# Kernel optimization log

Hardware: AMD Instinct MI355X
Metric: run time of the kernel (lower is better)

## Reference

```python
import jax, jax.numpy as jnp
import numpy as np

EPS = 1e-8
NEG_INF = -9e15  # matches torch masked_fill value


def setup_inputs() -> dict:
    key = jax.random.key(0)
    k1, k2 = jax.random.split(key)
    B, D = 4096, 512
    p1 = jax.random.normal(k1, (B, D), dtype=jnp.float32)
    p2 = jax.random.normal(k2, (B, D), dtype=jnp.float32)
    return {"p1": p1, "p2": p2}


def reference(p1, p2):
    # NT-Xent / InfoNCE loss as in SimCLR_MODEL.contrastive_loss (temperature = 1).
    z = jnp.concatenate([p1, p2], axis=0)              # [N, D], N = 2B
    # cosine similarity == GEMM of L2-normalized rows (torch eps clamp = 1e-8)
    zn = z / jnp.maximum(jnp.linalg.norm(z, axis=-1, keepdims=True), EPS)
    sim = zn @ zn.T                                     # [N, N]
    N = sim.shape[0]
    idx = jnp.arange(N)
    sim = sim.at[idx, idx].set(NEG_INF)                 # mask self-similarity
    # positive pair of row i is row (i + N/2) mod N (eye rolled by N/2)
    pos = sim[idx, (idx + N // 2) % N]                  # [N]
    nll = -pos + jax.nn.logsumexp(sim, axis=-1)
    return jnp.mean(nll)
```

## Files before the change

kernel.cpp:

```cpp
#include <hip/hip_runtime.h>
#include <hip/hip_bf16.h>
#include <math.h>

#define N_TOT 8192
#define HALF_N 4096
#define D_DIM 512
#define BM 128
#define BK 64
#define NTILES 2080

typedef float f32x4_t __attribute__((ext_vector_type(4)));

typedef __attribute__((address_space(1))) unsigned int g_u32;
typedef __attribute__((address_space(3))) unsigned int l_u32;

__global__ __launch_bounds__(256) void k_normalize(
    const float* __restrict__ p1, const float* __restrict__ p2,
    unsigned char* __restrict__ zf8, float* __restrict__ rowsum,
    float* __restrict__ out)
{
    const int w = threadIdx.x >> 6;
    const int lane = threadIdx.x & 63;
    const int row = blockIdx.x * 4 + w;

    if (threadIdx.x < 4) rowsum[blockIdx.x * 4 + threadIdx.x] = 0.0f;
    if (blockIdx.x == 0 && threadIdx.x == 0) out[0] = 0.0f;

    const float* src = (row < HALF_N) ? p1 + (size_t)row * D_DIM
                                      : p2 + (size_t)(row - HALF_N) * D_DIM;
    float4 a = *(const float4*)(src + lane * 4);
    float4 b = *(const float4*)(src + 256 + lane * 4);
    float s = a.x*a.x + a.y*a.y + a.z*a.z + a.w*a.w
            + b.x*b.x + b.y*b.y + b.z*b.z + b.w*b.w;
    #pragma unroll
    for (int m = 1; m < 64; m <<= 1) s += __shfl_xor(s, m, 64);
    float inv = 1.0f / fmaxf(sqrtf(s), 1e-8f);

    int pk0 = __builtin_amdgcn_cvt_pk_fp8_f32(a.x * inv, a.y * inv, 0, false);
    pk0     = __builtin_amdgcn_cvt_pk_fp8_f32(a.z * inv, a.w * inv, pk0, true);
    int pk1 = __builtin_amdgcn_cvt_pk_fp8_f32(b.x * inv, b.y * inv, 0, false);
    pk1     = __builtin_amdgcn_cvt_pk_fp8_f32(b.z * inv, b.w * inv, pk1, true);

    unsigned char* dst = zf8 + (size_t)row * D_DIM;
    *(int*)(dst + lane * 4) = pk0;
    *(int*)(dst + 256 + lane * 4) = pk1;
}

__global__ __launch_bounds__(256) void k_gemm(
    const unsigned char* __restrict__ zf8,
    float* __restrict__ rowsum, float* __restrict__ pos)
{
    __shared__ __align__(16) unsigned char As[BM * BK];
    __shared__ __align__(16) unsigned char Bs[BM * BK];

    const int tid = threadIdx.x;
    const int lane = tid & 63;
    const int w = tid >> 6;
    const int wr = w >> 1, wc = w & 1;
    const int q = lane >> 4, l15 = lane & 15;

    const int t = blockIdx.x;
    int bi = (int)((sqrtf(8.0f * (float)t + 1.0f) - 1.0f) * 0.5f);
    while ((bi + 1) * (bi + 2) / 2 <= t) ++bi;
    while (bi * (bi + 1) / 2 > t) --bi;
    const int bx = bi;
    const int by = t - bi * (bi + 1) / 2;
    const bool isDiag = (bx == by);
    const bool hasPos = (bx - by == 32);
    const int rowBase = by * BM;
    const int colBase = bx * BM;

    const int ci0 = tid;
    const int ci1 = 256 + tid;
    const int r0 = ci0 >> 2, cc0 = ci0 & 3;
    const int r1 = ci1 >> 2, cc1 = ci1 & 3;
    const int gc0 = cc0 ^ ((r0 >> 1) & 3);
    const int gc1 = cc1 ^ ((r1 >> 1) & 3);

    f32x4_t acc[4][4] = {};

    for (int kb = 0; kb < D_DIM; kb += BK) {
        const unsigned char* ga0 = zf8 + (size_t)(rowBase + r0) * D_DIM + kb + gc0 * 16;
        const unsigned char* ga1 = zf8 + (size_t)(rowBase + r1) * D_DIM + kb + gc1 * 16;
        const unsigned char* gb0 = zf8 + (size_t)(colBase + r0) * D_DIM + kb + gc0 * 16;
        const unsigned char* gb1 = zf8 + (size_t)(colBase + r1) * D_DIM + kb + gc1 * 16;
        __builtin_amdgcn_global_load_lds((const g_u32*)ga0, (l_u32*)&As[ci0 * 16], 16, 0, 0);
        __builtin_amdgcn_global_load_lds((const g_u32*)ga1, (l_u32*)&As[ci1 * 16], 16, 0, 0);
        __builtin_amdgcn_global_load_lds((const g_u32*)gb0, (l_u32*)&Bs[ci0 * 16], 16, 0, 0);
        __builtin_amdgcn_global_load_lds((const g_u32*)gb1, (l_u32*)&Bs[ci1 * 16], 16, 0, 0);
        __syncthreads();

        long long af[2][4], bfr[2][4];
        #pragma unroll
        for (int h = 0; h < 2; h++) {
            #pragma unroll
            for (int i = 0; i < 4; i++) {
                const int ra = wr * 64 + i * 16 + l15;
                const int rb = wc * 64 + i * 16 + l15;
                const int ca = ((h * 2 + (q >> 1)) ^ ((ra >> 1) & 3)) * 16 + (q & 1) * 8;
                const int cb = ((h * 2 + (q >> 1)) ^ ((rb >> 1) & 3)) * 16 + (q & 1) * 8;
                af[h][i]  = *(const long long*)&As[ra * BK + ca];
                bfr[h][i] = *(const long long*)&Bs[rb * BK + cb];
            }
        }
        #pragma unroll
        for (int h = 0; h < 2; h++)
            #pragma unroll
            for (int i = 0; i < 4; i++)
                #pragma unroll
                for (int j = 0; j < 4; j++)
                    acc[i][j] = __builtin_amdgcn_mfma_f32_16x16x32_fp8_fp8(
                        af[h][i], bfr[h][j], acc[i][j], 0, 0, 0);
        __syncthreads();
    }

    float colacc[4] = {0.f, 0.f, 0.f, 0.f};
    #pragma unroll
    for (int i = 0; i < 4; i++) {
        #pragma unroll
        for (int r = 0; r < 4; r++) {
            const int row = rowBase + wr * 64 + i * 16 + q * 4 + r;
            float rs = 0.0f;
            #pragma unroll
            for (int j = 0; j < 4; j++) {
                const int col = colBase + wc * 64 + j * 16 + l15;
                const float c = acc[i][j][r];
                float e = __expf(c);
                if (isDiag && col == row) e = 0.0f;
                rs += e;
                colacc[j] += e;
                if (hasPos && col == row + HALF_N) { pos[row] = c; pos[col] = c; }
            }
            rs += __shfl_xor(rs, 1); rs += __shfl_xor(rs, 2);
            rs += __shfl_xor(rs, 4); rs += __shfl_xor(rs, 8);
            if (l15 == 0) atomicAdd(&rowsum[row], rs);
        }
    }
    if (!isDiag) {
        #pragma unroll
        for (int j = 0; j < 4; j++) {
            float cs = colacc[j];
            cs += __shfl_xor(cs, 16);
            cs += __shfl_xor(cs, 32);
            if (q == 0) atomicAdd(&rowsum[colBase + wc * 64 + j * 16 + l15], cs);
        }
    }
}

__global__ __launch_bounds__(256) void k_finalize(
    const float* __restrict__ rowsum, const float* __restrict__ pos,
    float* __restrict__ out)
{
    const int t = threadIdx.x;
    const int i = blockIdx.x * 256 + t;
    float s = logf(rowsum[i]) - pos[i];
    #pragma unroll
    for (int m = 1; m < 64; m <<= 1) s += __shfl_xor(s, m, 64);
    __shared__ float red[4];
    if ((t & 63) == 0) red[t >> 6] = s;
    __syncthreads();
    if (t == 0)
        atomicAdd(out, (red[0] + red[1] + red[2] + red[3]) * (1.0f / (float)N_TOT));
}

extern "C" void kernel_launch(void* const* d_in, const int* in_sizes, int n_in,
                              void* d_out, int out_size, void* d_ws, size_t ws_size,
                              hipStream_t stream) {
    const float* p1 = (const float*)d_in[0];
    const float* p2 = (const float*)d_in[1];

    unsigned char* zf8 = (unsigned char*)d_ws;
    float* rowsum = (float*)((char*)d_ws + (size_t)N_TOT * D_DIM);
    float* pos    = rowsum + N_TOT;
    float* outp   = (float*)d_out;

    k_normalize<<<N_TOT / 4, 256, 0, stream>>>(p1, p2, zf8, rowsum, outp);
    k_gemm<<<NTILES, 256, 0, stream>>>(zf8, rowsum, pos);
    k_finalize<<<N_TOT / 256, 256, 0, stream>>>(rowsum, pos, outp);
}
```

Baseline: 109.2 us.

## Double-buffer LDS tiles in fp8 GEMM to prefetch the next K-slice

Splits the shared-memory A/B tiles into two buffers. The next K-slice is issued with global_load_lds while MFMAs run on the current slice, and one barrier per iteration replaces two. Precomputed base pointers and a fully unrolled K loop cut address arithmetic. launch_bounds(256,3) asks for three resident blocks per CU to help hide latency, which the doubled LDS use and register pressure could work against.

Result: no change. 108.9 us (-0.3%).

```diff
diff --git a/kernel.cpp b/kernel.cpp
--- a/kernel.cpp
+++ b/kernel.cpp
@@ -7,6 +7,7 @@
 #define D_DIM 512
 #define BM 128
 #define BK 64
+#define NKIT (D_DIM / BK)
 #define NTILES 2080
 
 typedef float f32x4_t __attribute__((ext_vector_type(4)));
@@ -46,12 +47,12 @@
     *(int*)(dst + 256 + lane * 4) = pk1;
 }
 
-__global__ __launch_bounds__(256) void k_gemm(
+__global__ __launch_bounds__(256, 3) void k_gemm(
     const unsigned char* __restrict__ zf8,
     float* __restrict__ rowsum, float* __restrict__ pos)
 {
-    __shared__ __align__(16) unsigned char As[BM * BK];
-    __shared__ __align__(16) unsigned char Bs[BM * BK];
+    __shared__ __align__(16) unsigned char As[2][BM * BK];
+    __shared__ __align__(16) unsigned char Bs[2][BM * BK];
 
     const int tid = threadIdx.x;
     const int lane = tid & 63;
@@ -77,18 +78,31 @@
     const int gc0 = cc0 ^ ((r0 >> 1) & 3);
     const int gc1 = cc1 ^ ((r1 >> 1) & 3);
 
+    const unsigned char* gA0 = zf8 + (size_t)(rowBase + r0) * D_DIM + gc0 * 16;
+    const unsigned char* gA1 = zf8 + (size_t)(rowBase + r1) * D_DIM + gc1 * 16;
+    const unsigned char* gB0 = zf8 + (size_t)(colBase + r0) * D_DIM + gc0 * 16;
+    const unsigned char* gB1 = zf8 + (size_t)(colBase + r1) * D_DIM + gc1 * 16;
+
     f32x4_t acc[4][4] = {};
 
-    for (int kb = 0; kb < D_DIM; kb += BK) {
-        const unsigned char* ga0 = zf8 + (size_t)(rowBase + r0) * D_DIM + kb + gc0 * 16;
-        const unsigned char* ga1 = zf8 + (size_t)(rowBase + r1) * D_DIM + kb + gc1 * 16;
-        const unsigned char* gb0 = zf8 + (size_t)(colBase + r0) * D_DIM + kb + gc0 * 16;
-        const unsigned char* gb1 = zf8 + (size_t)(colBase + r1) * D_DIM + kb + gc1 * 16;
-        __builtin_amdgcn_global_load_lds((const g_u32*)ga0, (l_u32*)&As[ci0 * 16], 16, 0, 0);
-        __builtin_amdgcn_global_load_lds((const g_u32*)ga1, (l_u32*)&As[ci1 * 16], 16, 0, 0);
-        __builtin_amdgcn_global_load_lds((const g_u32*)gb0, (l_u32*)&Bs[ci0 * 16], 16, 0, 0);
-        __builtin_amdgcn_global_load_lds((const g_u32*)gb1, (l_u32*)&Bs[ci1 * 16], 16, 0, 0);
+    __builtin_amdgcn_global_load_lds((const g_u32*)gA0, (l_u32*)&As[0][ci0 * 16], 16, 0, 0);
+    __builtin_amdgcn_global_load_lds((const g_u32*)gA1, (l_u32*)&As[0][ci1 * 16], 16, 0, 0);
+    __builtin_amdgcn_global_load_lds((const g_u32*)gB0, (l_u32*)&Bs[0][ci0 * 16], 16, 0, 0);
+    __builtin_amdgcn_global_load_lds((const g_u32*)gB1, (l_u32*)&Bs[0][ci1 * 16], 16, 0, 0);
+
+    #pragma unroll
+    for (int it = 0; it < NKIT; it++) {
+        const int cur = it & 1;
         __syncthreads();
+
+        if (it + 1 < NKIT) {
+            const int kb = (it + 1) * BK;
+            const int nxt = 1 - cur;
+            __builtin_amdgcn_global_load_lds((const g_u32*)(gA0 + kb), (l_u32*)&As[nxt][ci0 * 16], 16, 0, 0);
+            __builtin_amdgcn_global_load_lds((const g_u32*)(gA1 + kb), (l_u32*)&As[nxt][ci1 * 16], 16, 0, 0);
+            __builtin_amdgcn_global_load_lds((const g_u32*)(gB0 + kb), (l_u32*)&Bs[nxt][ci0 * 16], 16, 0, 0);
+            __builtin_amdgcn_global_load_lds((const g_u32*)(gB1 + kb), (l_u32*)&Bs[nxt][ci1 * 16], 16, 0, 0);
+        }
 
         long long af[2][4], bfr[2][4];
         #pragma unroll
@@ -99,8 +113,8 @@
                 const int rb = wc * 64 + i * 16 + l15;
                 const int ca = ((h * 2 + (q >> 1)) ^ ((ra >> 1) & 3)) * 16 + (q & 1) * 8;
                 const int cb = ((h * 2 + (q >> 1)) ^ ((rb >> 1) & 3)) * 16 + (q & 1) * 8;
-                af[h][i]  = *(const long long*)&As[ra * BK + ca];
-                bfr[h][i] = *(const long long*)&Bs[rb * BK + cb];
+                af[h][i]  = *(const long long*)&As[cur][ra * BK + ca];
+                bfr[h][i] = *(const long long*)&Bs[cur][rb * BK + cb];
             }
         }
         #pragma unroll
@@ -111,7 +125,6 @@
                 for (int j = 0; j < 4; j++)
                     acc[i][j] = __builtin_amdgcn_mfma_f32_16x16x32_fp8_fp8(
                         af[h][i], bfr[h][j], acc[i][j], 0, 0, 0);
-        __syncthreads();
     }
 
     float colacc[4] = {0.f, 0.f, 0.f, 0.f};
```

## Load MFMA fragments directly from global in pre-permuted fp8 layout, drop LDS staging

Applied to the files above, without the earlier changes.

The normalize kernel now writes fp8 rows in a permuted byte order within each 64-byte chunk, so each lane's two MFMA k-slices sit in one contiguous 16-byte run. The GEMM kernel drops shared memory and barriers and reads its A/B fragments straight from global memory with 16-byte vector loads, prefetching the next k-block in registers while the current one is multiplied. This removes LDS traffic and __syncthreads, but each wave now loads its own fragments, so data shared between waves is fetched redundantly through L1/L2 and register pressure goes up.

New measurement: 155.1 us. +41.9%, slower.

```diff
diff --git a/kernel.cpp b/kernel.cpp
--- a/kernel.cpp
+++ b/kernel.cpp
@@ -6,13 +6,11 @@
 #define HALF_N 4096
 #define D_DIM 512
 #define BM 128
-#define BK 64
+#define NKB 8
 #define NTILES 2080
 
 typedef float f32x4_t __attribute__((ext_vector_type(4)));
-
-typedef __attribute__((address_space(1))) unsigned int g_u32;
-typedef __attribute__((address_space(3))) unsigned int l_u32;
+typedef long long i64x2 __attribute__((ext_vector_type(2)));
 
 __global__ __launch_bounds__(256) void k_normalize(
     const float* __restrict__ p1, const float* __restrict__ p2,
@@ -42,17 +40,18 @@
     pk1     = __builtin_amdgcn_cvt_pk_fp8_f32(b.z * inv, b.w * inv, pk1, true);
 
     unsigned char* dst = zf8 + (size_t)row * D_DIM;
-    *(int*)(dst + lane * 4) = pk0;
-    *(int*)(dst + 256 + lane * 4) = pk1;
+    const int o0 = lane * 4;
+    const int o1 = 256 + lane * 4;
+    const int d0 = (o0 & ~63) + ((o0 >> 3) & 3) * 16 + ((o0 >> 5) & 1) * 8 + ((o0 >> 2) & 1) * 4;
+    const int d1 = (o1 & ~63) + ((o1 >> 3) & 3) * 16 + ((o1 >> 5) & 1) * 8 + ((o1 >> 2) & 1) * 4;
+    *(int*)(dst + d0) = pk0;
+    *(int*)(dst + d1) = pk1;
 }
 
 __global__ __launch_bounds__(256) void k_gemm(
     const unsigned char* __restrict__ zf8,
     float* __restrict__ rowsum, float* __restrict__ pos)
 {
-    __shared__ __align__(16) unsigned char As[BM * BK];
-    __shared__ __align__(16) unsigned char Bs[BM * BK];
-
     const int tid = threadIdx.x;
     const int lane = tid & 63;
     const int w = tid >> 6;
@@ -70,48 +69,47 @@
     const int rowBase = by * BM;
     const int colBase = bx * BM;
 
-    const int ci0 = tid;
-    const int ci1 = 256 + tid;
-    const int r0 = ci0 >> 2, cc0 = ci0 & 3;
-    const int r1 = ci1 >> 2, cc1 = ci1 & 3;
-    const int gc0 = cc0 ^ ((r0 >> 1) & 3);
-    const int gc1 = cc1 ^ ((r1 >> 1) & 3);
+    const unsigned char* aP[4];
+    const unsigned char* bP[4];
+    #pragma unroll
+    for (int i = 0; i < 4; i++) {
+        aP[i] = zf8 + (size_t)(rowBase + wr * 64 + i * 16 + l15) * D_DIM + q * 16;
+        bP[i] = zf8 + (size_t)(colBase + wc * 64 + i * 16 + l15) * D_DIM + q * 16;
+    }
 
     f32x4_t acc[4][4] = {};
 
-    for (int kb = 0; kb < D_DIM; kb += BK) {
-        const unsigned char* ga0 = zf8 + (size_t)(rowBase + r0) * D_DIM + kb + gc0 * 16;
-        const unsigned char* ga1 = zf8 + (size_t)(rowBase + r1) * D_DIM + kb + gc1 * 16;
-        const unsigned char* gb0 = zf8 + (size_t)(colBase + r0) * D_DIM + kb + gc0 * 16;
-        const unsigned char* gb1 = zf8 + (size_t)(colBase + r1) * D_DIM + kb + gc1 * 16;
-        __builtin_amdgcn_global_load_lds((const g_u32*)ga0, (l_u32*)&As[ci0 * 16], 16, 0, 0);
-        __builtin_amdgcn_global_load_lds((const g_u32*)ga1, (l_u32*)&As[ci1 * 16], 16, 0, 0);
-        __builtin_amdgcn_global_load_lds((const g_u32*)gb0, (l_u32*)&Bs[ci0 * 16], 16, 0, 0);
-        __builtin_amdgcn_global_load_lds((const g_u32*)gb1, (l_u32*)&Bs[ci1 * 16], 16, 0, 0);
-        __syncthreads();
+    i64x2 aCur[4], bCur[4];
+    #pragma unroll
+    for (int i = 0; i < 4; i++) {
+        aCur[i] = *(const i64x2*)(aP[i]);
+        bCur[i] = *(const i64x2*)(bP[i]);
+    }
 
-        long long af[2][4], bfr[2][4];
-        #pragma unroll
-        for (int h = 0; h < 2; h++) {
+    #pragma unroll
+    for (int b = 0; b < NKB; b++) {
+        i64x2 aNxt[4], bNxt[4];
+        if (b + 1 < NKB) {
+            const int off = (b + 1) * 64;
             #pragma unroll
             for (int i = 0; i < 4; i++) {
-                const int ra = wr * 64 + i * 16 + l15;
-                const int rb = wc * 64 + i * 16 + l15;
-                const int ca = ((h * 2 + (q >> 1)) ^ ((ra >> 1) & 3)) * 16 + (q & 1) * 8;
-                const int cb = ((h * 2 + (q >> 1)) ^ ((rb >> 1) & 3)) * 16 + (q & 1) * 8;
-                af[h][i]  = *(const long long*)&As[ra * BK + ca];
-                bfr[h][i] = *(const long long*)&Bs[rb * BK + cb];
+                aNxt[i] = *(const i64x2*)(aP[i] + off);
+                bNxt[i] = *(const i64x2*)(bP[i] + off);
             }
         }
         #pragma unroll
-        for (int h = 0; h < 2; h++)
+        for (int i = 0; i < 4; i++)
             #pragma unroll
-            for (int i = 0; i < 4; i++)
-                #pragma unroll
-                for (int j = 0; j < 4; j++)
-                    acc[i][j] = __builtin_amdgcn_mfma_f32_16x16x32_fp8_fp8(
-                        af[h][i], bfr[h][j], acc[i][j], 0, 0, 0);
-        __syncthreads();
+            for (int j = 0; j < 4; j++) {
+                acc[i][j] = __builtin_amdgcn_mfma_f32_16x16x32_fp8_fp8(
+                    aCur[i][0], bCur[j][0], acc[i][j], 0, 0, 0);
+                acc[i][j] = __builtin_amdgcn_mfma_f32_16x16x32_fp8_fp8(
+                    aCur[i][1], bCur[j][1], acc[i][j], 0, 0, 0);
+            }
+        if (b + 1 < NKB) {
+            #pragma unroll
+            for (int i = 0; i < 4; i++) { aCur[i] = aNxt[i]; bCur[i] = bNxt[i]; }
+        }
     }
 
     float colacc[4] = {0.f, 0.f, 0.f, 0.f};
```
